# Kernel optimization log

Measured on AMD Instinct MI355X. Metric: run time of the kernel, lower is better.

## Reference

```python
import jax, jax.numpy as jnp
import numpy as np

N, NPG, BS = 32000, 1000, 32
E, H, L, R, K = 512000, 128, 3, 8, 64


def setup_inputs() -> dict:
    key = jax.random.key(0)
    ks = jax.random.split(key, 16)
    sc = 0.05
    x = jax.random.normal(ks[0], (N, H), jnp.float32)
    W_rel = jax.random.normal(ks[1], (L, R, H, H), jnp.float32) * sc
    W_self = jax.random.normal(ks[2], (L, H, H), jnp.float32) * sc
    rel_table = jax.random.normal(ks[3], (R, H), jnp.float32)
    Zn = jax.random.normal(ks[4], (K, H), jnp.float32) * sc
    proj_W = jax.random.normal(ks[5], (L * H, H), jnp.float32) * sc
    proj_b = jnp.zeros((H,), jnp.float32)
    fc_W = jax.random.normal(ks[6], (2 * L * H + 2 * H, 1), jnp.float32) * sc
    fc_b = jnp.zeros((1,), jnp.float32)
    rep_seq = jax.random.normal(ks[7], (BS, H), jnp.float32)
    src = jax.random.randint(ks[8], (E,), 0, N, jnp.int32)
    dst = jax.random.randint(ks[9], (E,), 0, N, jnp.int32)
    etype = jax.random.randint(ks[10], (E,), 0, R, jnp.int32)
    graph_id = (jnp.arange(N, dtype=jnp.int32) // NPG).astype(jnp.int32)
    head_ids = (jnp.arange(BS, dtype=jnp.int32) * NPG)           # node with id==1 per subgraph
    tail_ids = (jnp.arange(BS, dtype=jnp.int32) * NPG + 1)       # node with id==2 per subgraph
    rel_labels = jax.random.randint(ks[11], (BS,), 0, R, jnp.int32)
    return dict(x=x, W_rel=W_rel, W_self=W_self, rel_table=rel_table, Zn=Zn,
                proj_W=proj_W, proj_b=proj_b, fc_W=fc_W, fc_b=fc_b, rep_seq=rep_seq,
                src=src, dst=dst, etype=etype, graph_id=graph_id,
                head_ids=head_ids, tail_ids=tail_ids, rel_labels=rel_labels)


def reference(x, W_rel, W_self, rel_table, Zn, proj_W, proj_b, fc_W, fc_b, rep_seq,
              src, dst, etype, graph_id, head_ids, tail_ids, rel_labels):
    n, h_dim = x.shape
    bs = head_ids.shape[0]
    # RGCN message passing: aggregate src features per (dst, rel), then per-rel linear.
    seg = dst.astype(jnp.int32) * R + etype.astype(jnp.int32)  # [E]
    h = x
    reprs = []
    for l in range(L):
        agg = jax.ops.segment_sum(h[src], seg, num_segments=n * R)  # [N*R, H]
        agg = agg.reshape(n, R, h_dim)
        msg = jnp.einsum('nri,rio->no', agg, W_rel[l])
        h = jax.nn.relu(msg + h @ W_self[l])
        reprs.append(h)
    repr_ = jnp.stack(reprs, axis=1)  # [N, L, H]
    # mean_nodes pooling per subgraph
    counts = jax.ops.segment_sum(jnp.ones((n,), x.dtype), graph_id, num_segments=bs)
    g_mean = jax.ops.segment_sum(repr_, graph_id, num_segments=bs) / counts[:, None, None]
    g_out = jax.nn.leaky_relu(g_mean.reshape(bs, L * h_dim) @ proj_W + proj_b)  # [bs, H]
    # head/tail gathers
    head_flat = repr_[head_ids].reshape(bs, L * h_dim)
    tail_flat = repr_[tail_ids].reshape(bs, L * h_dim)
    rel_embs = rel_table[rel_labels]  # [bs, H]
    h_out = head_flat @ proj_W + proj_b
    t_out = tail_flat @ proj_W + proj_b
    # community view: cluster assignment (softmax) then summary (sigmoid)
    s1 = jax.nn.sigmoid(jax.nn.softmax(h_out @ Zn.T, axis=-1) @ Zn)
    s2 = jax.nn.sigmoid(jax.nn.softmax(t_out @ Zn.T, axis=-1) @ Zn)
    s = s1 * s2
    # view attention aggregation over [subgraph, sequence, community] views
    views = jnp.stack([g_out, rep_seq, s], axis=1)  # [bs, 3, H]
    att = jax.nn.softmax(jnp.sum(rel_embs[:, None, :] * views, axis=-1), axis=-1)  # [bs, 3]
    view_aggr = jnp.sum(att[:, :, None] * views, axis=1)  # [bs, H]
    # positive triplet scoring
    g_rep = jnp.concatenate([head_flat, tail_flat, rel_embs, view_aggr], axis=1)
    out_pos = g_rep @ fc_W + fc_b  # [bs, 1]
    return out_pos
```

## Files before the change

kernel.cpp:

```cpp
#include <hip/hip_runtime.h>

#define N_NODES 32000
#define NPG     1000
#define BSZ     32
#define NEDGE   512000
#define H       128
#define NL      3
#define NR      8
#define NW      1152
#define NBIN    32768

typedef __attribute__((ext_vector_type(8))) short short8;
typedef __attribute__((ext_vector_type(4))) float float4v;

__device__ __forceinline__ float bf2f(unsigned short u) {
  union { unsigned int i; float f; } v;
  v.i = ((unsigned int)u) << 16;
  return v.f;
}
__device__ __forceinline__ unsigned short f2bf(float f) {
  union { float f; unsigned int i; } v;
  v.f = f;
  unsigned int x = v.i;
  return (unsigned short)((x + 0x7FFFu + ((x >> 16) & 1u)) >> 16);
}

__global__ __launch_bounds__(256) void k_prep(
    const float* __restrict__ x, const float* __restrict__ W_rel,
    const float* __restrict__ W_self, const int* __restrict__ dst,
    const int* __restrict__ graph_id,
    unsigned short* __restrict__ hb, unsigned short* __restrict__ Bt,
    int* __restrict__ cnt, int* __restrict__ gcount)
{
  const int b = blockIdx.x, t = threadIdx.x;
  if (b < 4000) {
    const size_t i = ((size_t)b * 256 + t) * 4;
    float4 v = *(const float4*)(x + i);
    ushort4 u = { f2bf(v.x), f2bf(v.y), f2bf(v.z), f2bf(v.w) };
    *(ushort4*)(hb + i) = u;
  } else if (b < 5728) {
    const int g = (b - 4000) * 256 + t;
    const int k = g & 127;
    const int n = (g >> 7) % NW;
    const int l = g / (NW * H);
    float v = (n < 1024) ? W_rel[(((size_t)l * NR + (n >> 7)) * H + k) * H + (n & 127)]
                         : W_self[((size_t)l * H + k) * H + (n - 1024)];
    Bt[(size_t)l * (NW * H) + (size_t)n * H + k] = f2bf(v);
  } else if (b < 7728) {
    const int e = (b - 5728) * 256 + t;
    atomicAdd(&cnt[dst[e]], 1);
  } else {
    __shared__ int hist[BSZ];
    if (t < BSZ) hist[t] = 0;
    __syncthreads();
    const int n = (b - 7728) * 256 + t;
    if (n < N_NODES) atomicAdd(&hist[graph_id[n]], 1);
    __syncthreads();
    if (t < BSZ) { int v = hist[t]; if (v) atomicAdd(&gcount[t], v); }
  }
}

__global__ __launch_bounds__(256) void k_scanA(const int* __restrict__ cnt,
                                               int* __restrict__ bsum) {
  __shared__ int red[256];
  const int t = threadIdx.x;
  int4 v = *(const int4*)(cnt + blockIdx.x * 1024 + t * 4);
  red[t] = v.x + v.y + v.z + v.w;
  __syncthreads();
  for (int off = 128; off > 0; off >>= 1) {
    if (t < off) red[t] += red[t + off];
    __syncthreads();
  }
  if (t == 0) bsum[blockIdx.x] = red[0];
}

__global__ __launch_bounds__(64) void k_scanB(const int* __restrict__ bsum,
                                              int* __restrict__ boff) {
  const int t = threadIdx.x;
  __shared__ int v[64];
  v[t] = (t < 32) ? bsum[t] : 0;
  __syncthreads();
  if (t == 0) {
    int r = 0;
    for (int i = 0; i < 32; ++i) { int c = v[i]; v[i] = r; r += c; }
  }
  __syncthreads();
  if (t < 32) boff[t] = v[t];
}

__global__ __launch_bounds__(256) void k_scanC(const int* __restrict__ cnt,
                                               const int* __restrict__ boff,
                                               int* __restrict__ row_ptr,
                                               int* __restrict__ cursor) {
  __shared__ int ts[256];
  const int t = threadIdx.x;
  const int base = blockIdx.x * 1024 + t * 4;
  int4 v = *(const int4*)(cnt + base);
  const int s = v.x + v.y + v.z + v.w;
  ts[t] = s;
  __syncthreads();
  for (int off = 1; off < 256; off <<= 1) {
    int val = (t >= off) ? ts[t - off] : 0;
    __syncthreads();
    ts[t] += val;
    __syncthreads();
  }
  int ex = ts[t] - s + boff[blockIdx.x];
  int4 w = { ex, ex + v.x, ex + v.x + v.y, ex + v.x + v.y + v.z };
  *(int4*)(row_ptr + base) = w;
  *(int4*)(cursor + base) = w;
}

__global__ void k_fill(const int* __restrict__ src, const int* __restrict__ dst,
                       const int* __restrict__ etype, int* __restrict__ cursor,
                       int* __restrict__ edge_off) {
  int e = blockIdx.x * blockDim.x + threadIdx.x;
  if (e < NEDGE) {
    int p = atomicAdd(&cursor[dst[e]], 1);
    edge_off[p] = src[e] * NW + etype[e] * H;
  }
}

__global__ __launch_bounds__(256) void k_gemm9(
    const unsigned short* __restrict__ Ah,
    const unsigned short* __restrict__ Bt,
    unsigned short* __restrict__ G)
{
  __shared__ unsigned short lds_a[128 * 136];
  __shared__ unsigned short lds_b[128 * 136];
  const int tid  = threadIdx.x;
  const int wave = tid >> 6, lane = tid & 63;
  const int l15 = lane & 15, quad = lane >> 4;
  const int m0 = blockIdx.x * 128;
  const int n0 = blockIdx.y * 128;
  const int mb = (wave & 1) * 64;
  const int nb = (wave >> 1) * 64;

  #pragma unroll
  for (int s = 0; s < 8; ++s) {
    int f  = s * 256 + tid;
    int m  = f >> 4;
    int ko = (f & 15) * 8;
    *(uint4*)(lds_a + m * 136 + ko) = *(const uint4*)(Ah + (size_t)(m0 + m) * H + ko);
    *(uint4*)(lds_b + m * 136 + ko) = *(const uint4*)(Bt + (size_t)(n0 + m) * H + ko);
  }
  __syncthreads();

  float4v acc[4][4];
  #pragma unroll
  for (int i = 0; i < 4; ++i)
    #pragma unroll
    for (int j = 0; j < 4; ++j) acc[i][j] = (float4v){0.f, 0.f, 0.f, 0.f};

  #pragma unroll
  for (int ks = 0; ks < 4; ++ks) {
    const int ko = ks * 32 + quad * 8;
    short8 afr[4], bfr[4];
    #pragma unroll
    for (int i = 0; i < 4; ++i)
      afr[i] = *(const short8*)(lds_a + (mb + i * 16 + l15) * 136 + ko);
    #pragma unroll
    for (int j = 0; j < 4; ++j)
      bfr[j] = *(const short8*)(lds_b + (nb + j * 16 + l15) * 136 + ko);
    #pragma unroll
    for (int i = 0; i < 4; ++i)
      #pragma unroll
      for (int j = 0; j < 4; ++j)
        acc[i][j] = __builtin_amdgcn_mfma_f32_16x16x32_bf16(afr[i], bfr[j], acc[i][j], 0, 0, 0);
  }

  __syncthreads();
  #pragma unroll
  for (int i = 0; i < 4; ++i)
    #pragma unroll
    for (int j = 0; j < 4; ++j)
      #pragma unroll
      for (int r = 0; r < 4; ++r)
        lds_a[(mb + i * 16 + quad * 4 + r) * 136 + nb + j * 16 + l15] = f2bf(acc[i][j][r]);
  __syncthreads();
  #pragma unroll
  for (int s = 0; s < 8; ++s) {
    int f  = s * 256 + tid;
    int m  = f >> 4;
    int ko = (f & 15) * 8;
    *(uint4*)(G + (size_t)(m0 + m) * NW + n0 + ko) = *(const uint4*)(lds_a + m * 136 + ko);
  }
}

__global__ __launch_bounds__(256) void k_gather(
    const unsigned short* __restrict__ G, const int* __restrict__ row_ptr,
    const int* __restrict__ edge_off, unsigned short* __restrict__ Hnext)
{
  const int node = blockIdx.x * 4 + (threadIdx.x >> 6);
  const int lane = threadIdx.x & 63;
  const int c0 = lane * 2;
  const int beg = row_ptr[node];
  const int end = row_ptr[node + 1];
  float sx, sy;
  {
    unsigned int u = *(const unsigned int*)(G + (size_t)node * NW + 1024 + c0);
    sx = bf2f((unsigned short)(u & 0xffff));
    sy = bf2f((unsigned short)(u >> 16));
  }
  int e = beg;
  for (; e + 8 <= end; e += 8) {
    int of[8]; unsigned int u[8];
    #pragma unroll
    for (int i = 0; i < 8; ++i) of[i] = edge_off[e + i];
    #pragma unroll
    for (int i = 0; i < 8; ++i)
      u[i] = *(const unsigned int*)(G + (size_t)of[i] + c0);
    #pragma unroll
    for (int i = 0; i < 8; ++i) {
      sx += bf2f((unsigned short)(u[i] & 0xffff));
      sy += bf2f((unsigned short)(u[i] >> 16));
    }
  }
  for (; e < end; ++e) {
    int of = edge_off[e];
    unsigned int u = *(const unsigned int*)(G + (size_t)of + c0);
    sx += bf2f((unsigned short)(u & 0xffff));
    sy += bf2f((unsigned short)(u >> 16));
  }
  sx = fmaxf(sx, 0.f);
  sy = fmaxf(sy, 0.f);
  *(unsigned int*)(Hnext + (size_t)node * H + c0) =
      (unsigned int)f2bf(sx) | ((unsigned int)f2bf(sy) << 16);
}

__global__ void k_gmean(const unsigned short* __restrict__ hb, float* __restrict__ gmean)
{
  const int g = blockIdx.x, l = blockIdx.y, c = blockIdx.z, t = threadIdx.x;
  const unsigned short* base =
      hb + ((size_t)(l + 1) * N_NODES + (size_t)g * NPG + (size_t)c * (NPG / 8)) * H + t * 2;
  float sx = 0.f, sy = 0.f;
  for (int i = 0; i < 125; ++i) {
    unsigned int u = *(const unsigned int*)(base + (size_t)i * H);
    sx += bf2f((unsigned short)(u & 0xffff));
    sy += bf2f((unsigned short)(u >> 16));
  }
  float* gp = gmean + (size_t)g * (NL * H) + l * H + t * 2;
  atomicAdd(gp, sx);
  atomicAdd(gp + 1, sy);
}

__global__ __launch_bounds__(128) void k_final(
    const unsigned short* __restrict__ hb, const float* __restrict__ gmean,
    const int* __restrict__ gcount,
    const float* __restrict__ rel_tb, const float* __restrict__ Zn,
    const float* __restrict__ projW, const float* __restrict__ projB,
    const float* __restrict__ fcW, const float* __restrict__ fcB,
    const float* __restrict__ repSeq,
    const int* __restrict__ head_ids, const int* __restrict__ tail_ids,
    const int* __restrict__ rel_lab, float* __restrict__ out)
{
  const int b = blockIdx.x;
  const int o = threadIdx.x;
  __shared__ float gm[384], hf[384], tf[384];
  __shared__ float go[128], ho[128], t_o[128], re[128], rs[128], sv[128];
  __shared__ float lg[128], pr[128], red[128], att[3];

  const int hid = head_ids[b], tlid = tail_ids[b], rl = rel_lab[b];
  const float cinv = 1.f / (float)gcount[b];
  #pragma unroll
  for (int l = 0; l < NL; ++l) {
    gm[l * H + o] = gmean[(size_t)b * (NL * H) + l * H + o] * cinv;
    hf[l * H + o] = bf2f(hb[((size_t)(l + 1) * N_NODES + hid) * H + o]);
    tf[l * H + o] = bf2f(hb[((size_t)(l + 1) * N_NODES + tlid) * H + o]);
  }
  re[o] = rel_tb[rl * H + o];
  rs[o] = repSeq[b * H + o];
  __syncthreads();

  float pb = projB[o];
  float sg = pb, sh = pb, st = pb;
  for (int i = 0; i < NL * H; ++i) {
    float wv = projW[i * H + o];
    sg = fmaf(gm[i], wv, sg);
    sh = fmaf(hf[i], wv, sh);
    st = fmaf(tf[i], wv, st);
  }
  go[o] = (sg > 0.f) ? sg : 0.01f * sg;
  ho[o] = sh;
  t_o[o] = st;
  __syncthreads();

  {
    const int k = o & 63;
    const float* v = (o < 64) ? ho : t_o;
    float s = 0.f;
    for (int i = 0; i < H; ++i) s = fmaf(v[i], Zn[k * H + i], s);
    lg[o] = s;
  }
  __syncthreads();
  if (o < 2) {
    float* l0 = &lg[o * 64];
    float* p0 = &pr[o * 64];
    float mx = l0[0];
    for (int k = 1; k < 64; ++k) mx = fmaxf(mx, l0[k]);
    float sum = 0.f;
    for (int k = 0; k < 64; ++k) { float e = __expf(l0[k] - mx); p0[k] = e; sum += e; }
    float inv = 1.f / sum;
    for (int k = 0; k < 64; ++k) p0[k] *= inv;
  }
  __syncthreads();
  {
    float s1 = 0.f, s2 = 0.f;
    for (int k = 0; k < 64; ++k) {
      float z = Zn[k * H + o];
      s1 = fmaf(pr[k], z, s1);
      s2 = fmaf(pr[64 + k], z, s2);
    }
    s1 = 1.f / (1.f + __expf(-s1));
    s2 = 1.f / (1.f + __expf(-s2));
    sv[o] = s1 * s2;
  }
  __syncthreads();
  if (o == 0) {
    float d0 = 0.f, d1 = 0.f, d2 = 0.f;
    for (int i = 0; i < H; ++i) { d0 += re[i] * go[i]; d1 += re[i] * rs[i]; d2 += re[i] * sv[i]; }
    float mx = fmaxf(d0, fmaxf(d1, d2));
    float e0 = __expf(d0 - mx), e1 = __expf(d1 - mx), e2 = __expf(d2 - mx);
    float inv = 1.f / (e0 + e1 + e2);
    att[0] = e0 * inv; att[1] = e1 * inv; att[2] = e2 * inv;
  }
  __syncthreads();
  float va = att[0] * go[o] + att[1] * rs[o] + att[2] * sv[o];

  float p = 0.f;
  p = fmaf(hf[o],       fcW[o],       p);
  p = fmaf(hf[128 + o], fcW[128 + o], p);
  p = fmaf(hf[256 + o], fcW[256 + o], p);
  p = fmaf(tf[o],       fcW[384 + o], p);
  p = fmaf(tf[128 + o], fcW[512 + o], p);
  p = fmaf(tf[256 + o], fcW[640 + o], p);
  p = fmaf(re[o],       fcW[768 + o], p);
  p = fmaf(va,          fcW[896 + o], p);
  red[o] = p;
  __syncthreads();
  if (o == 0) {
    float s = 0.f;
    for (int i = 0; i < 128; ++i) s += red[i];
    out[b] = s + fcB[0];
  }
}

extern "C" void kernel_launch(void* const* d_in, const int* in_sizes, int n_in,
                              void* d_out, int out_size, void* d_ws, size_t ws_size,
                              hipStream_t stream) {
  const float* x        = (const float*)d_in[0];
  const float* W_rel    = (const float*)d_in[1];
  const float* W_self   = (const float*)d_in[2];
  const float* rel_tb   = (const float*)d_in[3];
  const float* Zn       = (const float*)d_in[4];
  const float* proj_W   = (const float*)d_in[5];
  const float* proj_b   = (const float*)d_in[6];
  const float* fc_W     = (const float*)d_in[7];
  const float* fc_b     = (const float*)d_in[8];
  const float* rep_seq  = (const float*)d_in[9];
  const int* src      = (const int*)d_in[10];
  const int* dst      = (const int*)d_in[11];
  const int* etype    = (const int*)d_in[12];
  const int* graph_id = (const int*)d_in[13];
  const int* head_ids = (const int*)d_in[14];
  const int* tail_ids = (const int*)d_in[15];
  const int* rel_lab  = (const int*)d_in[16];
  float* out = (float*)d_out;

  char* w = (char*)d_ws;
  unsigned short* G  = (unsigned short*)w; w += (size_t)N_NODES * NW * 2;
  unsigned short* hb = (unsigned short*)w; w += (size_t)(NL + 1) * N_NODES * H * 2;
  unsigned short* Bt = (unsigned short*)w; w += (size_t)NL * NW * H * 2;
  int* row_ptr  = (int*)w;  w += (size_t)NBIN * 4;
  int* edge_off = (int*)w;  w += (size_t)NEDGE * 4;
  int* bsum     = (int*)w;  w += (size_t)64 * 4;
  int* boff     = (int*)w;  w += (size_t)64 * 4;
  char* z = w;
  int* cursor  = (int*)w;   w += (size_t)NBIN * 4;
  int* gcount  = (int*)w;   w += (size_t)32 * 4;
  float* gmean = (float*)w; w += (size_t)BSZ * NL * H * 4;
  size_t zbytes = (size_t)(w - z);

  hipMemsetAsync(z, 0, zbytes, stream);
  k_prep <<<7853, 256, 0, stream>>>(x, W_rel, W_self, dst, graph_id, hb, Bt, cursor, gcount);
  k_scanA<<<NBIN / 1024, 256, 0, stream>>>(cursor, bsum);
  k_scanB<<<1, 64, 0, stream>>>(bsum, boff);
  k_scanC<<<NBIN / 1024, 256, 0, stream>>>(cursor, boff, row_ptr, cursor);
  k_fill <<<NEDGE / 256, 256, 0, stream>>>(src, dst, etype, cursor, edge_off);

  for (int l = 0; l < NL; ++l) {
    const unsigned short* hp = hb + (size_t)l * N_NODES * H;
    unsigned short* hn = hb + (size_t)(l + 1) * N_NODES * H;
    k_gemm9 <<<dim3(N_NODES / 128, 9), 256, 0, stream>>>(hp, Bt + (size_t)l * NW * H, G);
    k_gather<<<N_NODES / 4, 256, 0, stream>>>(G, row_ptr, edge_off, hn);
  }
  k_gmean<<<dim3(BSZ, NL, 8), 64, 0, stream>>>(hb, gmean);
  k_final<<<BSZ, H, 0, stream>>>(hb, gmean, gcount, rel_tb, Zn, proj_W, proj_b, fc_W, fc_b,
                                 rep_seq, head_ids, tail_ids, rel_lab, out);
  (void)in_sizes; (void)n_in; (void)out_size; (void)ws_size;
}
```

Baseline: 352.8 us.

## Merge three scan kernels into one block; widen gather loads to 8 bytes

The three-kernel prefix scan (block sums, offsets, final scan) becomes a single 1024-thread block in which each thread scans 32 counts, removing two launches. The edge gather now has each 64-lane wave split into two halves that take alternating edges, each lane loading 4 bf16 values (uint2), and the halves are combined with a cross-half shuffle. This aims to cut launch overhead and raise bytes per load in the memory-bound gather, at the cost of a serial single-block scan and half the lanes idle for the self-term and the store.

```diff
diff --git a/kernel.cpp b/kernel.cpp
--- a/kernel.cpp
+++ b/kernel.cpp
@@ -60,55 +60,36 @@
   }
 }
 
-__global__ __launch_bounds__(256) void k_scanA(const int* __restrict__ cnt,
-                                               int* __restrict__ bsum) {
-  __shared__ int red[256];
+__global__ __launch_bounds__(1024) void k_scan1(const int* __restrict__ cnt,
+                                                int* __restrict__ row_ptr,
+                                                int* __restrict__ cursor) {
+  __shared__ int lds[1024];
   const int t = threadIdx.x;
-  int4 v = *(const int4*)(cnt + blockIdx.x * 1024 + t * 4);
-  red[t] = v.x + v.y + v.z + v.w;
-  __syncthreads();
-  for (int off = 128; off > 0; off >>= 1) {
-    if (t < off) red[t] += red[t + off];
+  const int base = t * 32;
+  int v[32];
+  #pragma unroll
+  for (int i = 0; i < 8; ++i)
+    *(int4*)(v + i * 4) = *(const int4*)(cnt + base + i * 4);
+  int s = 0;
+  #pragma unroll
+  for (int i = 0; i < 32; ++i) s += v[i];
+  lds[t] = s;
+  __syncthreads();
+  for (int off = 1; off < 1024; off <<= 1) {
+    int val = (t >= off) ? lds[t - off] : 0;
     __syncthreads();
-  }
-  if (t == 0) bsum[blockIdx.x] = red[0];
-}
-
-__global__ __launch_bounds__(64) void k_scanB(const int* __restrict__ bsum,
-                                              int* __restrict__ boff) {
-  const int t = threadIdx.x;
-  __shared__ int v[64];
-  v[t] = (t < 32) ? bsum[t] : 0;
-  __syncthreads();
-  if (t == 0) {
-    int r = 0;
-    for (int i = 0; i < 32; ++i) { int c = v[i]; v[i] = r; r += c; }
-  }
-  __syncthreads();
-  if (t < 32) boff[t] = v[t];
-}
-
-__global__ __launch_bounds__(256) void k_scanC(const int* __restrict__ cnt,
-                                               const int* __restrict__ boff,
-                                               int* __restrict__ row_ptr,
-                                               int* __restrict__ cursor) {
-  __shared__ int ts[256];
-  const int t = threadIdx.x;
-  const int base = blockIdx.x * 1024 + t * 4;
-  int4 v = *(const int4*)(cnt + base);
-  const int s = v.x + v.y + v.z + v.w;
-  ts[t] = s;
-  __syncthreads();
-  for (int off = 1; off < 256; off <<= 1) {
-    int val = (t >= off) ? ts[t - off] : 0;
+    lds[t] += val;
     __syncthreads();
-    ts[t] += val;
-    __syncthreads();
-  }
-  int ex = ts[t] - s + boff[blockIdx.x];
-  int4 w = { ex, ex + v.x, ex + v.x + v.y, ex + v.x + v.y + v.z };
-  *(int4*)(row_ptr + base) = w;
-  *(int4*)(cursor + base) = w;
+  }
+  int run = lds[t] - s;
+  int w[32];
+  #pragma unroll
+  for (int i = 0; i < 32; ++i) { w[i] = run; run += v[i]; }
+  #pragma unroll
+  for (int i = 0; i < 8; ++i) {
+    *(int4*)(row_ptr + base + i * 4) = *(int4*)(w + i * 4);
+    *(int4*)(cursor  + base + i * 4) = *(int4*)(w + i * 4);
+  }
 }
 
 __global__ void k_fill(const int* __restrict__ src, const int* __restrict__ dst,
@@ -193,39 +174,50 @@
 {
   const int node = blockIdx.x * 4 + (threadIdx.x >> 6);
   const int lane = threadIdx.x & 63;
-  const int c0 = lane * 2;
+  const int half = lane >> 5;
+  const int li   = lane & 31;
+  const int c0   = li * 4;
   const int beg = row_ptr[node];
   const int end = row_ptr[node + 1];
-  float sx, sy;
-  {
-    unsigned int u = *(const unsigned int*)(G + (size_t)node * NW + 1024 + c0);
-    sx = bf2f((unsigned short)(u & 0xffff));
-    sy = bf2f((unsigned short)(u >> 16));
-  }
-  int e = beg;
-  for (; e + 8 <= end; e += 8) {
-    int of[8]; unsigned int u[8];
-    #pragma unroll
-    for (int i = 0; i < 8; ++i) of[i] = edge_off[e + i];
-    #pragma unroll
-    for (int i = 0; i < 8; ++i)
-      u[i] = *(const unsigned int*)(G + (size_t)of[i] + c0);
-    #pragma unroll
-    for (int i = 0; i < 8; ++i) {
-      sx += bf2f((unsigned short)(u[i] & 0xffff));
-      sy += bf2f((unsigned short)(u[i] >> 16));
-    }
-  }
-  for (; e < end; ++e) {
-    int of = edge_off[e];
-    unsigned int u = *(const unsigned int*)(G + (size_t)of + c0);
-    sx += bf2f((unsigned short)(u & 0xffff));
-    sy += bf2f((unsigned short)(u >> 16));
-  }
-  sx = fmaxf(sx, 0.f);
-  sy = fmaxf(sy, 0.f);
-  *(unsigned int*)(Hnext + (size_t)node * H + c0) =
-      (unsigned int)f2bf(sx) | ((unsigned int)f2bf(sy) << 16);
+  float s0 = 0.f, s1 = 0.f, s2 = 0.f, s3 = 0.f;
+  if (half == 0) {
+    uint2 u = *(const uint2*)(G + (size_t)node * NW + 1024 + c0);
+    s0 = bf2f((unsigned short)(u.x & 0xffff));
+    s1 = bf2f((unsigned short)(u.x >> 16));
+    s2 = bf2f((unsigned short)(u.y & 0xffff));
+    s3 = bf2f((unsigned short)(u.y >> 16));
+  }
+#define ACC4(u) { \
+    s0 += bf2f((unsigned short)((u).x & 0xffff)); \
+    s1 += bf2f((unsigned short)((u).x >> 16));    \
+    s2 += bf2f((unsigned short)((u).y & 0xffff)); \
+    s3 += bf2f((unsigned short)((u).y >> 16)); }
+  int e = beg + half;
+  for (; e + 6 < end; e += 8) {
+    int o0 = edge_off[e],     o1 = edge_off[e + 2];
+    int o2 = edge_off[e + 4], o3 = edge_off[e + 6];
+    uint2 u0 = *(const uint2*)(G + o0 + c0);
+    uint2 u1 = *(const uint2*)(G + o1 + c0);
+    uint2 u2 = *(const uint2*)(G + o2 + c0);
+    uint2 u3 = *(const uint2*)(G + o3 + c0);
+    ACC4(u0) ACC4(u1) ACC4(u2) ACC4(u3)
+  }
+  for (; e < end; e += 2) {
+    int o = edge_off[e];
+    uint2 u = *(const uint2*)(G + o + c0);
+    ACC4(u)
+  }
+#undef ACC4
+  s0 += __shfl_xor(s0, 32);
+  s1 += __shfl_xor(s1, 32);
+  s2 += __shfl_xor(s2, 32);
+  s3 += __shfl_xor(s3, 32);
+  if (half == 0) {
+    uint2 w;
+    w.x = (unsigned int)f2bf(fmaxf(s0, 0.f)) | ((unsigned int)f2bf(fmaxf(s1, 0.f)) << 16);
+    w.y = (unsigned int)f2bf(fmaxf(s2, 0.f)) | ((unsigned int)f2bf(fmaxf(s3, 0.f)) << 16);
+    *(uint2*)(Hnext + (size_t)node * H + c0) = w;
+  }
 }
 
 __global__ void k_gmean(const unsigned short* __restrict__ hb, float* __restrict__ gmean)
@@ -373,8 +365,6 @@
   unsigned short* Bt = (unsigned short*)w; w += (size_t)NL * NW * H * 2;
   int* row_ptr  = (int*)w;  w += (size_t)NBIN * 4;
   int* edge_off = (int*)w;  w += (size_t)NEDGE * 4;
-  int* bsum     = (int*)w;  w += (size_t)64 * 4;
-  int* boff     = (int*)w;  w += (size_t)64 * 4;
   char* z = w;
   int* cursor  = (int*)w;   w += (size_t)NBIN * 4;
   int* gcount  = (int*)w;   w += (size_t)32 * 4;
@@ -383,9 +373,7 @@
 
   hipMemsetAsync(z, 0, zbytes, stream);
   k_prep <<<7853, 256, 0, stream>>>(x, W_rel, W_self, dst, graph_id, hb, Bt, cursor, gcount);
-  k_scanA<<<NBIN / 1024, 256, 0, stream>>>(cursor, bsum);
-  k_scanB<<<1, 64, 0, stream>>>(bsum, boff);
-  k_scanC<<<NBIN / 1024, 256, 0, stream>>>(cursor, boff, row_ptr, cursor);
+  k_scan1<<<1, 1024, 0, stream>>>(cursor, row_ptr, cursor);
   k_fill <<<NEDGE / 256, 256, 0, stream>>>(src, dst, etype, cursor, edge_off);
 
   for (int l = 0; l < NL; ++l) {
```

Result: no change. 351.3 us (-0.4%).
